# Performance work log

Measured on AMD Instinct MI355X. Metric: run time of the kernel, lower is better.

The kernel has to match this reference:

```python
import jax, jax.numpy as jnp
import numpy as np

L, H, NH, HD, F, B, S = 32, 1024, 16, 64, 2048, 2, 2048
HPH = H // NH  # hidden per attention head (hyena column split)
EPS = 1e-6
BLOCK = {0:'HCS',4:'HCS',7:'HCS',11:'HCS',14:'HCS',18:'HCS',21:'HCS',25:'HCS',28:'HCS',
         1:'HCM',5:'HCM',8:'HCM',12:'HCM',15:'HCM',19:'HCM',22:'HCM',26:'HCM',29:'HCM',
         2:'HCL',6:'HCL',9:'HCL',13:'HCL',16:'HCL',20:'HCL',23:'HCL',27:'HCL',30:'HCL',
         3:'ATT',10:'ATT',17:'ATT',24:'ATT',31:'ATT'}

def rmsnorm(x, w):
    return x * jax.lax.rsqrt(jnp.mean(x * x, -1, keepdims=True) + EPS) * w

def step_fir(u, state, w, b, flip=False, gated=False):
    # u:[B,C]  state:[B,C,cache]  w:[C,Lf]  b:[C]  (single-token FIR step)
    cache = state.shape[-1]
    w = w[:, ::-1][:, -(cache + 1):] if flip else w[:, :cache + 1]
    y = w[:, -1] * u + jnp.sum(state * w[:, :-1], -1)
    y = y + (b * u if gated else b)
    return y

def split3(z):
    # column_split_hyena=True path of _interleave_split
    r = z.reshape(z.shape[0], NH, 3 * HPH)
    x2 = r[:, :, :HPH].reshape(z.shape[0], H)
    x1 = r[:, :, HPH:2 * HPH].reshape(z.shape[0], H)
    v = r[:, :, 2 * HPH:].reshape(z.shape[0], H)
    return x2, x1, v

def mlp(x, W1, W2):
    return jax.nn.gelu(x @ W1.T) @ W2.T

def fir_block(x, n1, n2, pW, pb, oW, ob, W1, W2, sfw, sfb, h, D, fstate, istate, flip, gated):
    xn = rmsnorm(x, n1)
    z = xn @ pW.T + pb                 # [B,1,3H]
    u = z[:, -1]                       # [B,3H]
    zp = step_fir(u, fstate, sfw, sfb)
    x2, x1, v = split3(zp)
    y = step_fir(x1 * v, istate, h, D, flip=flip, gated=gated)
    y = (y * x2)[:, None]              # [B,1,H]
    x = y @ oW.T + ob + x
    return mlp(rmsnorm(x, n2), W1, W2) + x

def hcl_block(x, n1, n2, pW, pb, oW, ob, W1, W2, sfw, sfb, log_poles, residues, D, fstate, iir):
    xn = rmsnorm(x, n1)
    z = xn @ pW.T + pb
    u = z[:, -1]
    zp = step_fir(u, fstate, sfw, sfb)
    x2, x1, v = split3(zp)
    x1v = x1 * v
    iir_new = jnp.exp(log_poles) * iir + x1v[..., None]   # [B,H,SS] single-step IIR update
    res = jnp.sum(residues * iir_new, -1)
    y = (x2 * (res + D * x1v))[:, None]
    x = y @ oW.T + ob + x
    return mlp(rmsnorm(x, n2), W1, W2) + x

def att_block(x, n1, n2, qW, qb, oW, ob, W1, W2, kc, vc, cos, sin, pos):
    xn = rmsnorm(x, n1)
    qkv = (xn @ qW.T + qb).reshape(B, 1, 3, NH, HD)
    q, k, v = qkv[:, :, 0], qkv[:, :, 1], qkv[:, :, 2]
    c = jnp.concatenate([cos[pos], cos[pos]])  # [HD]
    s = jnp.concatenate([sin[pos], sin[pos]])
    rot = lambda t: jnp.concatenate([-t[..., HD // 2:], t[..., :HD // 2]], -1)
    q = q * c + rot(q) * s
    k = k * c + rot(k) * s
    kc = kc.at[:, pos].set(k[:, 0])  # KV-cache scatter write at current position
    vc = vc.at[:, pos].set(v[:, 0])
    scores = jnp.einsum('bohd,bshd->bhos', q, kc) * (HD ** -0.5)
    scores = jnp.where(jnp.arange(S) > pos, -10000.0, scores)
    aw = jax.nn.softmax(scores, -1)
    ctx = jnp.einsum('bhos,bshd->bohd', aw, vc).reshape(B, 1, H)
    x = ctx @ oW.T + ob + x
    return mlp(rmsnorm(x, n2), W1, W2) + x

def forward(x, position, norm1_w, norm2_w, proj_W, proj_b, out_W, out_b, mlp_W1, mlp_W2,
            sf_w, sf_b, hcs_h, hcs_D, hcm_h, hcm_D, hcl_logpoles, hcl_residues, hcl_D,
            fir_state, hcs_state, hcm_state, iir_state, k_cache, v_cache, rope_cos, rope_sin):
    att = 0
    for i in range(L):  # loop over 32 structurally distinct layers (static)
        t = BLOCK[i]
        cm = (norm1_w[i], norm2_w[i], proj_W[i], proj_b[i], out_W[i], out_b[i], mlp_W1[i], mlp_W2[i])
        if t == 'HCS':
            x = fir_block(x, *cm, sf_w[i], sf_b[i], hcs_h[i], hcs_D[i], fir_state[i], hcs_state[i], False, False)
        elif t == 'HCM':
            x = fir_block(x, *cm, sf_w[i], sf_b[i], hcm_h[i], hcm_D[i], fir_state[i], hcm_state[i], True, True)
        elif t == 'HCL':
            x = hcl_block(x, *cm, sf_w[i], sf_b[i], hcl_logpoles[i], hcl_residues[i], hcl_D[i], fir_state[i], iir_state[i])
        else:
            x = att_block(x, *cm, k_cache[att], v_cache[att], rope_cos, rope_sin, position)
            att += 1
    return x

def setup_inputs():
    key = jax.random.key(0)
    ks = jax.random.split(key, 24)
    g = lambda k, shape, sc: jax.random.normal(k, shape, jnp.float32) * sc
    inv_freq = 1.0 / (10000.0 ** (np.arange(0, HD, 2, dtype=np.float32) / HD))
    ang = np.arange(S, dtype=np.float32)[:, None] * inv_freq[None, :]
    return {
        'x': g(ks[0], (B, 1, H), 1.0),
        'position': 1024,
        'norm1_w': jnp.ones((L, H), jnp.float32),
        'norm2_w': jnp.ones((L, H), jnp.float32),
        'proj_W': g(ks[1], (L, 3 * H, H), H ** -0.5),
        'proj_b': jnp.zeros((L, 3 * H), jnp.float32),
        'out_W': g(ks[2], (L, H, H), 0.2 * H ** -0.5),
        'out_b': jnp.zeros((L, H), jnp.float32),
        'mlp_W1': g(ks[3], (L, F, H), H ** -0.5),
        'mlp_W2': g(ks[4], (L, H, F), 0.2 * F ** -0.5),
        'sf_w': g(ks[5], (L, 3 * H, 3), 0.4),
        'sf_b': g(ks[6], (L, 3 * H), 0.02),
        'hcs_h': g(ks[7], (L, H, 7), 0.2),
        'hcs_D': g(ks[8], (L, H), 0.2),
        'hcm_h': g(ks[9], (L, H, 128), 0.04),
        'hcm_D': g(ks[10], (L, H), 0.2),
        'hcl_logpoles': -jax.random.uniform(ks[11], (L, H, 16), jnp.float32, 0.01, 2.0),
        'hcl_residues': g(ks[12], (L, H, 16), 0.1),
        'hcl_D': g(ks[13], (L, H), 0.2),
        'fir_state': g(ks[14], (L, B, 3 * H, 2), 0.5),
        'hcs_state': g(ks[15], (L, B, H, 6), 0.5),
        'hcm_state': g(ks[16], (L, B, H, 127), 0.5),
        'iir_state': g(ks[17], (L, B, H, 16), 0.5),
        'k_cache': g(ks[18], (5, B, S, NH, HD), 1.0),
        'v_cache': g(ks[19], (5, B, S, NH, HD), 1.0),
        'rope_cos': jnp.asarray(np.cos(ang)),
        'rope_sin': jnp.asarray(np.sin(ang)),
    }

def reference(x, position, norm1_w, norm2_w, proj_W, proj_b, out_W, out_b, mlp_W1, mlp_W2,
              sf_w, sf_b, hcs_h, hcs_D, hcm_h, hcm_D, hcl_logpoles, hcl_residues, hcl_D,
              fir_state, hcs_state, hcm_state, iir_state, k_cache, v_cache, rope_cos, rope_sin):
    return forward(x, position, norm1_w, norm2_w, proj_W, proj_b, out_W, out_b, mlp_W1, mlp_W2,
                   sf_w, sf_b, hcs_h, hcs_D, hcm_h, hcm_D, hcl_logpoles, hcl_residues, hcl_D,
                   fir_state, hcs_state, hcm_state, iir_state, k_cache, v_cache, rope_cos, rope_sin)
```

## Files before the change

kernel.cpp:

```cpp
#include <hip/hip_runtime.h>
#include <hip/hip_bf16.h>
#include <math.h>

#define LAYERS 32
#define H      1024
#define H3     3072
#define NHEADS 16
#define HDIM   64
#define FF     2048
#define BATCH  2
#define SEQ    2048
#define EPSF   1e-6f

__device__ __forceinline__ float wredSum(float v) {
#pragma unroll
  for (int m = 32; m >= 1; m >>= 1) v += __shfl_xor(v, m, 64);
  return v;
}
__device__ __forceinline__ float wredMax(float v) {
#pragma unroll
  for (int m = 32; m >= 1; m >>= 1) v = fmaxf(v, __shfl_xor(v, m, 64));
  return v;
}
__device__ __forceinline__ float gelu_t(float x) {
  return 0.5f * x * (1.0f + tanhf(0.7978845608028654f * (x + 0.044715f * x * x * x)));
}
__device__ __forceinline__ float dot4(float4 a, float4 b) {
  return a.x * b.x + a.y * b.y + a.z * b.z + a.w * b.w;
}

__device__ __forceinline__ void ast(float* p, float v) {
  __hip_atomic_store(p, v, __ATOMIC_RELAXED, __HIP_MEMORY_SCOPE_AGENT);
}
__device__ __forceinline__ float ald(const float* p) {
  return __hip_atomic_load(p, __ATOMIC_RELAXED, __HIP_MEMORY_SCOPE_AGENT);
}
union F2U { unsigned long long u; float f[2]; };
__device__ __forceinline__ void ast2(unsigned long long* p, float lo, float hi) {
  F2U x; x.f[0] = lo; x.f[1] = hi;
  __hip_atomic_store(p, x.u, __ATOMIC_RELAXED, __HIP_MEMORY_SCOPE_AGENT);
}
__device__ __forceinline__ float2 ald2(const unsigned long long* p) {
  F2U x; x.u = __hip_atomic_load(p, __ATOMIC_RELAXED, __HIP_MEMORY_SCOPE_AGENT);
  return make_float2(x.f[0], x.f[1]);
}

__device__ __forceinline__ void slot_mark(int* slots, int idx) {
  __syncthreads();
  if (threadIdx.x == 0)
    __hip_atomic_store(&slots[idx], 1, __ATOMIC_RELAXED, __HIP_MEMORY_SCOPE_AGENT);
}
__device__ __forceinline__ void leader_detect(int* slots, int n, int* flags) {
  for (int s = threadIdx.x; s < n; s += 256) {
    while (__hip_atomic_load(&slots[s], __ATOMIC_RELAXED, __HIP_MEMORY_SCOPE_AGENT) == 0)
      __builtin_amdgcn_s_sleep(2);
  }
  __syncthreads();
  if (threadIdx.x < 8)
    __hip_atomic_store(&flags[threadIdx.x * 16], 1, __ATOMIC_RELAXED, __HIP_MEMORY_SCOPE_AGENT);
  asm volatile("" ::: "memory");
}
__device__ __forceinline__ void flag_wait(int* flags, int bid) {
  if (threadIdx.x == 0) {
    while (__hip_atomic_load(&flags[(bid & 7) * 16], __ATOMIC_RELAXED, __HIP_MEMORY_SCOPE_AGENT) == 0)
      __builtin_amdgcn_s_sleep(8);
  }
  __syncthreads();
  asm volatile("" ::: "memory");
}

union SH2 {
  struct { float xe[2048]; float red[8]; } ns;
  struct { float ys[2048]; float sml[512]; } mx;
  struct { float hs[4096]; } w2;
  struct { float q[64]; float k[64]; float v[64]; float eg[256]; float redA[4]; float osum[4][64]; } att;
};

__global__ __launch_bounds__(256, 6) void layer_k(
    int kind,
    const float* __restrict__ xin, float* __restrict__ xout,
    const float* __restrict__ n1L, const float* __restrict__ n2L,
    const float* __restrict__ pWL, const float* __restrict__ pbL,
    const float* __restrict__ oWL, const float* __restrict__ obL,
    const float* __restrict__ W1L, const float* __restrict__ W2L,
    const float* __restrict__ sfcL, const float* __restrict__ sfdL,
    const float* __restrict__ mix0L, const float* __restrict__ mix1L,
    const float* __restrict__ kcL, const float* __restrict__ vcL,
    const int* __restrict__ posp,
    const float* __restrict__ cosT, const float* __restrict__ sinT,
    unsigned long long* __restrict__ z2, float* __restrict__ attP,
    unsigned long long* __restrict__ xM2, unsigned long long* __restrict__ h2,
    int* __restrict__ barL)
{
  __shared__ SH2 sh;
  int bid = blockIdx.x, tid = threadIdx.x, lane = tid & 63, w = tid >> 6;
  int mixBase = (kind == 3) ? 1024 : 768;
  int w1Base  = (kind == 3) ? 1280 : 1024;
  int w2Base  = w1Base + 512;

  if (bid < 768) {
    float4 xv0 = ((const float4*)xin)[tid];
    float4 xv1 = ((const float4*)xin)[tid + 256];
    float4 nv  = ((const float4*)n1L)[tid];
    int r = bid * 4 + w;
    const float4* rowp = (const float4*)(pWL + (size_t)r * H);
    float4 wv0 = rowp[lane], wv1 = rowp[lane + 64],
           wv2 = rowp[lane + 128], wv3 = rowp[lane + 192];

    float ss0 = dot4(xv0, xv0), ss1 = dot4(xv1, xv1);
    ((float4*)sh.ns.xe)[tid]       = make_float4(xv0.x * nv.x, xv0.y * nv.y, xv0.z * nv.z, xv0.w * nv.w);
    ((float4*)sh.ns.xe)[tid + 256] = make_float4(xv1.x * nv.x, xv1.y * nv.y, xv1.z * nv.z, xv1.w * nv.w);
    ss0 = wredSum(ss0); ss1 = wredSum(ss1);
    if (lane == 0) { sh.ns.red[w] = ss0; sh.ns.red[4 + w] = ss1; }
    __syncthreads();
    float s0 = rsqrtf((sh.ns.red[0] + sh.ns.red[1] + sh.ns.red[2] + sh.ns.red[3]) * (1.0f / H) + EPSF);
    float s1 = rsqrtf((sh.ns.red[4] + sh.ns.red[5] + sh.ns.red[6] + sh.ns.red[7]) * (1.0f / H) + EPSF);

    const float4* x4 = (const float4*)sh.ns.xe;
    float a0 = dot4(wv0, x4[lane])       + dot4(wv1, x4[lane + 64])
             + dot4(wv2, x4[lane + 128]) + dot4(wv3, x4[lane + 192]);
    float a1 = dot4(wv0, x4[lane + 256]) + dot4(wv1, x4[lane + 320])
             + dot4(wv2, x4[lane + 384]) + dot4(wv3, x4[lane + 448]);
    a0 = wredSum(a0); a1 = wredSum(a1);
    if (lane == 0) {
      float b0 = pbL[r];
      ast2(&z2[r], a0 * s0 + b0, a1 * s1 + b0);
    }
    slot_mark(barL, bid);

  } else if (kind == 3 && bid < 1024) {
    int mb = bid - 768;
    int sp = mb & 7, n = (mb >> 3) & 15, b = mb >> 7;
    int pos = *posp;
    if (mb == 0) leader_detect(barL, 768, barL + 3072);
    else         flag_wait(barL + 3072, bid);
    if (tid < 64) {
      int d = tid, j = d & 31;
      float cs = cosT[pos * 32 + j], sn = sinT[pos * 32 + j];
      float2 zq  = ald2(&z2[n * 64 + d]);
      float2 zqo = ald2(&z2[n * 64 + ((d + 32) & 63)]);
      float2 zk  = ald2(&z2[1024 + n * 64 + d]);
      float2 zko = ald2(&z2[1024 + n * 64 + ((d + 32) & 63)]);
      float2 zv  = ald2(&z2[2048 + n * 64 + d]);
      float qv = b ? zq.y : zq.x,  qo = b ? zqo.y : zqo.x;
      float kv = b ? zk.y : zk.x,  ko = b ? zko.y : zko.x;
      sh.att.q[d] = ((d < 32) ? (qv * cs - qo * sn) : (qv * cs + qo * sn)) * 0.125f;
      sh.att.k[d] = (d < 32) ? (kv * cs - ko * sn) : (kv * cs + ko * sn);
      sh.att.v[d] = b ? zv.y : zv.x;
    }
    __syncthreads();
    int s = sp * 256 + tid;
    float logit = -1e30f;
    if (s <= pos) {
      const float4* k4 = (s == pos) ? (const float4*)sh.att.k
                                    : (const float4*)(kcL + (((size_t)b * SEQ + s) * NHEADS + n) * HDIM);
      const float4* q4 = (const float4*)sh.att.q;
      float acc = 0.f;
#pragma unroll
      for (int j = 0; j < 16; j++) acc += dot4(k4[j], q4[j]);
      logit = acc;
    }
    float m = wredMax(logit);
    if (lane == 0) sh.att.redA[w] = m;
    __syncthreads();
    m = fmaxf(fmaxf(sh.att.redA[0], sh.att.redA[1]), fmaxf(sh.att.redA[2], sh.att.redA[3]));
    float e = (s <= pos) ? expf(logit - m) : 0.f;
    sh.att.eg[tid] = e;
    float ps = wredSum(e);
    __syncthreads();
    if (lane == 0) sh.att.redA[w] = ps;
    __syncthreads();
    float lsum = sh.att.redA[0] + sh.att.redA[1] + sh.att.redA[2] + sh.att.redA[3];

    int dgrp = lane & 15, srow = lane >> 4;
    float4 acc = make_float4(0.f, 0.f, 0.f, 0.f);
#pragma unroll 4
    for (int it = 0; it < 16; it++) {
      int sl = w * 64 + it * 4;
      if (sp * 256 + sl > pos) break;
      int sli = sl + srow;
      int ss2 = sp * 256 + sli;
      float ev = sh.att.eg[sli];
      const float4* v4 = (ss2 == pos) ? (const float4*)sh.att.v
                                      : (const float4*)(vcL + (((size_t)b * SEQ + ss2) * NHEADS + n) * HDIM);
      float4 vv = v4[dgrp];
      acc.x += ev * vv.x; acc.y += ev * vv.y; acc.z += ev * vv.z; acc.w += ev * vv.w;
    }
#pragma unroll
    for (int mm = 16; mm <= 32; mm <<= 1) {
      acc.x += __shfl_xor(acc.x, mm, 64);
      acc.y += __shfl_xor(acc.y, mm, 64);
      acc.z += __shfl_xor(acc.z, mm, 64);
      acc.w += __shfl_xor(acc.w, mm, 64);
    }
    if (srow == 0) ((float4*)sh.att.osum[w])[dgrp] = acc;
    __syncthreads();
    float* Pp = attP + (size_t)((sp * BATCH + b) * NHEADS + n) * 66;
    if (tid < 64) ast(&Pp[tid], sh.att.osum[0][tid] + sh.att.osum[1][tid] + sh.att.osum[2][tid] + sh.att.osum[3][tid]);
    if (tid == 64) ast(&Pp[64], m);
    if (tid == 65) ast(&Pp[65], lsum);
    slot_mark(barL + 1024, mb);

  } else if (bid < w1Base) {
    int mb = bid - mixBase;
    int r = mb * 4 + w;
    const float4* rowp = (const float4*)(oWL + (size_t)r * H);
    float4 wv0 = rowp[lane], wv1 = rowp[lane + 64],
           wv2 = rowp[lane + 128], wv3 = rowp[lane + 192];

    if (kind != 3) {
      if (mb == 0) leader_detect(barL, 768, barL + 3200);
      else         flag_wait(barL + 3200, bid);
#pragma unroll
      for (int k = 0; k < 4; k++) {
        int c = tid + k * 256;
        int n = c >> 6, d = c & 63;
        int base = n * 192 + d;
        float2 za = ald2(&z2[base]);
        float2 zb = ald2(&z2[base + 64]);
        float2 zc = ald2(&z2[base + 128]);
        float x2a = sfcL[base] * za.x + sfdL[base];
        float x2b = sfcL[base] * za.y + sfdL[H3 + base];
        float x1a = sfcL[base + 64] * zb.x + sfdL[base + 64];
        float x1b = sfcL[base + 64] * zb.y + sfdL[H3 + base + 64];
        float va  = sfcL[base + 128] * zc.x + sfdL[base + 128];
        float vb  = sfcL[base + 128] * zc.y + sfdL[H3 + base + 128];
        sh.mx.ys[c]        = (mix1L[c] * (x1a * va) + mix0L[c]) * x2a;
        sh.mx.ys[1024 + c] = (mix1L[c] * (x1b * vb) + mix0L[H + c]) * x2b;
      }
    } else {
      if (mb == 0) leader_detect(barL + 1024, 256, barL + 3200);
      else         flag_wait(barL + 3200, bid);
      if (tid < 256) {
        int sp = tid & 7, n = (tid >> 3) & 15, b = tid >> 7;
        const float* Pp = attP + (size_t)((sp * BATCH + b) * NHEADS + n) * 66;
        sh.mx.sml[tid * 2] = ald(&Pp[64]);
        sh.mx.sml[tid * 2 + 1] = ald(&Pp[65]);
      }
      __syncthreads();
#pragma unroll
      for (int it = 0; it < 8; it++) {
        int e = tid + it * 256;
        int b = e >> 10, c = e & 1023;
        int n = c >> 6, d = c & 63;
        float M = -1e30f;
#pragma unroll
        for (int sp = 0; sp < 8; sp++) M = fmaxf(M, sh.mx.sml[(((b << 4) | n) * 8 + sp) * 2]);
        float Ls = 0.f, num = 0.f;
#pragma unroll
        for (int sp = 0; sp < 8; sp++) {
          float Msp = sh.mx.sml[(((b << 4) | n) * 8 + sp) * 2];
          float Lsp = sh.mx.sml[(((b << 4) | n) * 8 + sp) * 2 + 1];
          float wgt = expf(Msp - M);
          Ls += wgt * Lsp;
          num += wgt * ald(&attP[(size_t)((sp * BATCH + b) * NHEADS + n) * 66 + d]);
        }
        sh.mx.ys[e] = num / Ls;
      }
    }
    __syncthreads();
    const float4* y4 = (const float4*)sh.mx.ys;
    float a0 = dot4(wv0, y4[lane])       + dot4(wv1, y4[lane + 64])
             + dot4(wv2, y4[lane + 128]) + dot4(wv3, y4[lane + 192]);
    float a1 = dot4(wv0, y4[lane + 256]) + dot4(wv1, y4[lane + 320])
             + dot4(wv2, y4[lane + 384]) + dot4(wv3, y4[lane + 448]);
    a0 = wredSum(a0); a1 = wredSum(a1);
    if (lane == 0) {
      ast2(&xM2[r], a0 + obL[r] + xin[r], a1 + obL[r] + xin[H + r]);
    }
    slot_mark(barL + 1536, mb);

  } else if (bid < w2Base) {
    int wb = bid - w1Base;
    int r = wb * 4 + w;
    const float4* rowp = (const float4*)(W1L + (size_t)r * H);
    float4 wv0 = rowp[lane], wv1 = rowp[lane + 64],
           wv2 = rowp[lane + 128], wv3 = rowp[lane + 192];
    if (wb == 0) leader_detect(barL + 1536, 256, barL + 3328);
    else         flag_wait(barL + 3328, bid);

    float ss0 = 0.f, ss1 = 0.f;
#pragma unroll
    for (int k = 0; k < 4; k++) {
      int c = tid + k * 256;
      float2 xv = ald2(&xM2[c]);
      ss0 += xv.x * xv.x; ss1 += xv.y * xv.y;
      float nvj = n2L[c];
      sh.ns.xe[c] = xv.x * nvj;
      sh.ns.xe[1024 + c] = xv.y * nvj;
    }
    ss0 = wredSum(ss0); ss1 = wredSum(ss1);
    if (lane == 0) { sh.ns.red[w] = ss0; sh.ns.red[4 + w] = ss1; }
    __syncthreads();
    float s0 = rsqrtf((sh.ns.red[0] + sh.ns.red[1] + sh.ns.red[2] + sh.ns.red[3]) * (1.0f / H) + EPSF);
    float s1 = rsqrtf((sh.ns.red[4] + sh.ns.red[5] + sh.ns.red[6] + sh.ns.red[7]) * (1.0f / H) + EPSF);

    const float4* x4 = (const float4*)sh.ns.xe;
    float a0 = dot4(wv0, x4[lane])       + dot4(wv1, x4[lane + 64])
             + dot4(wv2, x4[lane + 128]) + dot4(wv3, x4[lane + 192]);
    float a1 = dot4(wv0, x4[lane + 256]) + dot4(wv1, x4[lane + 320])
             + dot4(wv2, x4[lane + 384]) + dot4(wv3, x4[lane + 448]);
    a0 = wredSum(a0); a1 = wredSum(a1);
    if (lane == 0) {
      ast2(&h2[r], gelu_t(a0 * s0), gelu_t(a1 * s1));
    }
    slot_mark(barL + 2048, wb);

  } else {
    int vb = bid - w2Base;
    int r = vb * 4 + w;
    const float4* rowp = (const float4*)(W2L + (size_t)r * FF);
    float4 wv[8];
#pragma unroll
    for (int j = 0; j < 8; j++) wv[j] = rowp[lane + 64 * j];
    if (vb == 0) leader_detect(barL + 2048, 512, barL + 3456);
    else         flag_wait(barL + 3456, bid);
#pragma unroll
    for (int it = 0; it < 8; it++) {
      int e = tid + it * 256;
      float2 hv = ald2(&h2[e]);
      sh.w2.hs[e] = hv.x;
      sh.w2.hs[2048 + e] = hv.y;
    }
    __syncthreads();
    const float4* h4 = (const float4*)sh.w2.hs;
    float a0 = 0.f, a1 = 0.f;
#pragma unroll
    for (int j = 0; j < 8; j++) {
      a0 += dot4(wv[j], h4[lane + 64 * j]);
      a1 += dot4(wv[j], h4[lane + 64 * j + 512]);
    }
    a0 = wredSum(a0); a1 = wredSum(a1);
    if (lane == 0) {
      float2 xm = ald2(&xM2[r]);
      xout[r]     = a0 + xm.x;
      xout[H + r] = a1 + xm.y;
    }
  }
}

__global__ __launch_bounds__(256) void prep_kernel(
    const float* __restrict__ sf_w, const float* __restrict__ sf_b,
    const float* __restrict__ fir_state,
    const float* __restrict__ hcs_h, const float* __restrict__ hcs_D, const float* __restrict__ hcs_state,
    const float* __restrict__ hcm_h, const float* __restrict__ hcm_D, const float* __restrict__ hcm_state,
    const float* __restrict__ lp, const float* __restrict__ resd, const float* __restrict__ hcl_D,
    const float* __restrict__ iir,
    unsigned long long kbits,
    float* __restrict__ sfd, float* __restrict__ sfc,
    float* __restrict__ mix0, float* __restrict__ mix1, int* __restrict__ bar)
{
  int blk = blockIdx.x, tid = threadIdx.x;
  if (blk < 768) {
    int idx = blk * 256 + tid;
    int i = idx / (BATCH * H3);
    int r = idx % (BATCH * H3);
    int b = r / H3, ch = r % H3;
    const float* fs = fir_state + ((size_t)(i * BATCH + b) * H3 + ch) * 2;
    const float* sw = sf_w + ((size_t)i * H3 + ch) * 3;
    sfd[idx] = fs[0] * sw[0] + fs[1] * sw[1] + sf_b[i * H3 + ch];
    if (b == 0) sfc[i * H3 + ch] = sw[2];
  } else if (blk < 1024) {
    int idx = (blk - 768) * 256 + tid;
    int i = idx >> 11;
    int r = idx & 2047;
    int b = r >> 10, c = r & 1023;
    int kind = (int)((kbits >> (2 * i)) & 3ull);
    if (kind == 0) {
      const float* st = hcs_state + ((size_t)(i * BATCH + b) * H + c) * 6;
      const float* hh = hcs_h + ((size_t)i * H + c) * 7;
      float acc = 0.f;
#pragma unroll
      for (int k = 0; k < 6; k++) acc += st[k] * hh[k];
      mix0[idx] = acc + hcs_D[i * H + c];
      if (b == 0) mix1[i * H + c] = hh[6];
    } else if (kind == 2) {
      const float* ii = iir + ((size_t)(i * BATCH + b) * H + c) * 16;
      const float* lpp = lp + ((size_t)i * H + c) * 16;
      const float* rs = resd + ((size_t)i * H + c) * 16;
      float acc = 0.f, rsum = 0.f;
#pragma unroll
      for (int k = 0; k < 16; k++) { float rv = rs[k]; acc += rv * expf(lpp[k]) * ii[k]; rsum += rv; }
      mix0[idx] = acc;
      if (b == 0) mix1[i * H + c] = rsum + hcl_D[i * H + c];
    }
  } else if (blk < 5632) {
    int w = tid >> 6, lane = tid & 63;
    int widx = (blk - 1024) * 4 + w;
    if (widx < 9 * BATCH * H) {
      int li = widx >> 11;
      int r = widx & 2047;
      int b = r >> 10, c = r & 1023;
      int i = (li >> 1) * 7 + ((li & 1) ? 5 : 1);
      const float* st = hcm_state + ((size_t)(i * BATCH + b) * H + c) * 127;
      const float* hh = hcm_h + ((size_t)i * H + c) * 128;
      float acc = 0.f;
      int k = lane;
      if (k < 127) acc += st[k] * hh[127 - k];
      k = lane + 64;
      if (k < 127) acc += st[k] * hh[127 - k];
      acc = wredSum(acc);
      if (lane == 0) {
        mix0[(i * BATCH + b) * H + c] = acc;
        if (b == 0) mix1[i * H + c] = hh[0] + hcm_D[i * H + c];
      }
    }
  } else {
    int idx = (blk - 5632) * 256 + tid;
    if (idx < LAYERS * 4096) bar[idx] = 0;
  }
}

extern "C" void kernel_launch(void* const* d_in, const int* in_sizes, int n_in,
                              void* d_out, int out_size, void* d_ws, size_t ws_size,
                              hipStream_t stream) {
  (void)in_sizes; (void)n_in; (void)out_size; (void)ws_size;
  const float* x0    = (const float*)d_in[0];
  const int*   posp  = (const int*)d_in[1];
  const float* n1    = (const float*)d_in[2];
  const float* n2    = (const float*)d_in[3];
  const float* pW    = (const float*)d_in[4];
  const float* pb    = (const float*)d_in[5];
  const float* oW    = (const float*)d_in[6];
  const float* ob    = (const float*)d_in[7];
  const float* W1    = (const float*)d_in[8];
  const float* W2    = (const float*)d_in[9];
  const float* sfw   = (const float*)d_in[10];
  const float* sfb   = (const float*)d_in[11];
  const float* hcs_h = (const float*)d_in[12];
  const float* hcs_D = (const float*)d_in[13];
  const float* hcm_h = (const float*)d_in[14];
  const float* hcm_D = (const float*)d_in[15];
  const float* lp    = (const float*)d_in[16];
  const float* resd  = (const float*)d_in[17];
  const float* hclD  = (const float*)d_in[18];
  const float* fir   = (const float*)d_in[19];
  const float* hcsS  = (const float*)d_in[20];
  const float* hcmS  = (const float*)d_in[21];
  const float* iir   = (const float*)d_in[22];
  const float* kc    = (const float*)d_in[23];
  const float* vc    = (const float*)d_in[24];
  const float* cosT  = (const float*)d_in[25];
  const float* sinT  = (const float*)d_in[26];

  float* ws    = (float*)d_ws;
  float* xbuf0 = ws;
  float* xbuf1 = ws + 2048;
  unsigned long long* xM2 = (unsigned long long*)(ws + 4096);
  unsigned long long* z2  = (unsigned long long*)(ws + 6144);
  unsigned long long* h2  = (unsigned long long*)(ws + 12288);
  float* attP  = ws + 16384;
  float* sfd   = ws + 33280;
  float* sfc   = ws + 229888;
  float* mix0  = ws + 328192;
  float* mix1  = ws + 393728;
  int*   bar   = (int*)(ws + 426496);

  static const int KIND[LAYERS] = {0,1,2,3,0,1,2,0,1,2,3,0,1,2,0,1,2,3,0,1,2,0,1,2,3,0,1,2,0,1,2,3};
  unsigned long long kbits = 0ull;
  for (int i = 0; i < LAYERS; i++) kbits |= ((unsigned long long)KIND[i]) << (2 * i);

  prep_kernel<<<6144, 256, 0, stream>>>(sfw, sfb, fir, hcs_h, hcs_D, hcsS,
      hcm_h, hcm_D, hcmS, lp, resd, hclD, iir, kbits, sfd, sfc, mix0, mix1, bar);

  const float* xsrc = x0;
  int att = 0;
  for (int i = 0; i < LAYERS; i++) {
    int kind = KIND[i];
    int nb = (kind == 3) ? 2048 : 1792;
    float* xout = (i == LAYERS - 1) ? (float*)d_out : ((i & 1) ? xbuf1 : xbuf0);
    const float* kcL = (kind == 3) ? kc + (size_t)att * BATCH * SEQ * NHEADS * HDIM : kc;
    const float* vcL = (kind == 3) ? vc + (size_t)att * BATCH * SEQ * NHEADS * HDIM : vc;
    layer_k<<<nb, 256, 0, stream>>>(
        kind, xsrc, xout,
        n1 + i * H, n2 + i * H,
        pW + (size_t)i * H3 * H, pb + i * H3,
        oW + (size_t)i * H * H, ob + i * H,
        W1 + (size_t)i * FF * H, W2 + (size_t)i * H * FF,
        sfc + (size_t)i * H3, sfd + (size_t)i * BATCH * H3,
        mix0 + (size_t)i * BATCH * H, mix1 + (size_t)i * H,
        kcL, vcL, posp, cosT, sinT,
        z2, attP, xM2, h2, bar + (size_t)i * 4096);
    if (kind == 3) att++;
    xsrc = xout;
  }
}
```

Before: 739.9 us.

## Fuse all 32 per-layer launches into one persistent mega-kernel with flag chaining

Replaces the host loop of 32 layer_k launches with a single launch of 32×2048 blocks. Each block derives its layer and kind from its block index. Layers are chained through device-side flags, so each layer's projection stage waits for the previous layer's W2 stage to finish. The residual stream is passed through ping-pong 64-bit interleaved buffers using atomic loads and stores. This removes per-launch overhead and lets weight rows for the next layer load before the dependency wait, overlapping memory traffic across layer boundaries. The costs are spinning waiter blocks that occupy CU slots, idle early-exit blocks in non-attention layers, and reliance on in-order block dispatch to avoid deadlock.

```diff
diff --git a/kernel.cpp b/kernel.cpp
--- a/kernel.cpp
+++ b/kernel.cpp
@@ -76,46 +76,62 @@
   struct { float q[64]; float k[64]; float v[64]; float eg[256]; float redA[4]; float osum[4][64]; } att;
 };
 
-__global__ __launch_bounds__(256, 6) void layer_k(
-    int kind,
-    const float* __restrict__ xin, float* __restrict__ xout,
-    const float* __restrict__ n1L, const float* __restrict__ n2L,
-    const float* __restrict__ pWL, const float* __restrict__ pbL,
-    const float* __restrict__ oWL, const float* __restrict__ obL,
-    const float* __restrict__ W1L, const float* __restrict__ W2L,
-    const float* __restrict__ sfcL, const float* __restrict__ sfdL,
-    const float* __restrict__ mix0L, const float* __restrict__ mix1L,
-    const float* __restrict__ kcL, const float* __restrict__ vcL,
-    const int* __restrict__ posp,
+__global__ __launch_bounds__(256, 8) void mega(
+    const float* __restrict__ x0, const int* __restrict__ posp,
+    const float* __restrict__ n1, const float* __restrict__ n2,
+    const float* __restrict__ pW, const float* __restrict__ pb,
+    const float* __restrict__ oW, const float* __restrict__ ob,
+    const float* __restrict__ W1, const float* __restrict__ W2,
+    const float* __restrict__ sfc, const float* __restrict__ sfd,
+    const float* __restrict__ mix0, const float* __restrict__ mix1,
+    const float* __restrict__ kc, const float* __restrict__ vc,
     const float* __restrict__ cosT, const float* __restrict__ sinT,
     unsigned long long* __restrict__ z2, float* __restrict__ attP,
     unsigned long long* __restrict__ xM2, unsigned long long* __restrict__ h2,
-    int* __restrict__ barL)
+    unsigned long long* __restrict__ xqA, unsigned long long* __restrict__ xqB,
+    int* __restrict__ bar, float* __restrict__ dout)
 {
   __shared__ SH2 sh;
   int bid = blockIdx.x, tid = threadIdx.x, lane = tid & 63, w = tid >> 6;
-  int mixBase = (kind == 3) ? 1024 : 768;
-  int w1Base  = (kind == 3) ? 1280 : 1024;
-  int w2Base  = w1Base + 512;
-
-  if (bid < 768) {
-    float4 xv0 = ((const float4*)xin)[tid];
-    float4 xv1 = ((const float4*)xin)[tid + 256];
-    float4 nv  = ((const float4*)n1L)[tid];
-    int r = bid * 4 + w;
-    const float4* rowp = (const float4*)(pWL + (size_t)r * H);
+  int layer = bid >> 11, local = bid & 2047;
+  int r7 = layer % 7;
+  int kind = (r7 == 3) ? 3 : ((r7 == 0 || r7 == 4) ? 0 : ((r7 == 1 || r7 == 5) ? 1 : 2));
+  int* barL = bar + layer * 4096;
+  unsigned long long* xr = (layer & 1) ? xqA : xqB;
+  unsigned long long* xw = (layer & 1) ? xqB : xqA;
+
+  if (local < 768) {
+    int r = local * 4 + w;
+    const float4* rowp = (const float4*)(pW + (size_t)layer * H3 * H + (size_t)r * H);
     float4 wv0 = rowp[lane], wv1 = rowp[lane + 64],
            wv2 = rowp[lane + 128], wv3 = rowp[lane + 192];
-
-    float ss0 = dot4(xv0, xv0), ss1 = dot4(xv1, xv1);
-    ((float4*)sh.ns.xe)[tid]       = make_float4(xv0.x * nv.x, xv0.y * nv.y, xv0.z * nv.z, xv0.w * nv.w);
-    ((float4*)sh.ns.xe)[tid + 256] = make_float4(xv1.x * nv.x, xv1.y * nv.y, xv1.z * nv.z, xv1.w * nv.w);
+    float4 nv = ((const float4*)(n1 + (size_t)layer * H))[tid];
+    if (layer > 0) {
+      if (local == 0) leader_detect(bar + (layer - 1) * 4096 + 2560, 256, barL + 3584);
+      else            flag_wait(barL + 3584, local);
+    }
+    float ss0 = 0.f, ss1 = 0.f;
+    if (layer == 0) {
+      float4 xv0 = ((const float4*)x0)[tid];
+      float4 xv1 = ((const float4*)x0)[tid + 256];
+      ss0 = dot4(xv0, xv0); ss1 = dot4(xv1, xv1);
+      ((float4*)sh.ns.xe)[tid]       = make_float4(xv0.x * nv.x, xv0.y * nv.y, xv0.z * nv.z, xv0.w * nv.w);
+      ((float4*)sh.ns.xe)[tid + 256] = make_float4(xv1.x * nv.x, xv1.y * nv.y, xv1.z * nv.z, xv1.w * nv.w);
+    } else {
+      float nn[4] = {nv.x, nv.y, nv.z, nv.w};
+#pragma unroll
+      for (int j = 0; j < 4; j++) {
+        float2 v = ald2(&xr[4 * tid + j]);
+        ss0 += v.x * v.x; ss1 += v.y * v.y;
+        sh.ns.xe[4 * tid + j] = v.x * nn[j];
+        sh.ns.xe[1024 + 4 * tid + j] = v.y * nn[j];
+      }
+    }
     ss0 = wredSum(ss0); ss1 = wredSum(ss1);
     if (lane == 0) { sh.ns.red[w] = ss0; sh.ns.red[4 + w] = ss1; }
     __syncthreads();
     float s0 = rsqrtf((sh.ns.red[0] + sh.ns.red[1] + sh.ns.red[2] + sh.ns.red[3]) * (1.0f / H) + EPSF);
     float s1 = rsqrtf((sh.ns.red[4] + sh.ns.red[5] + sh.ns.red[6] + sh.ns.red[7]) * (1.0f / H) + EPSF);
-
     const float4* x4 = (const float4*)sh.ns.xe;
     float a0 = dot4(wv0, x4[lane])       + dot4(wv1, x4[lane + 64])
              + dot4(wv2, x4[lane + 128]) + dot4(wv3, x4[lane + 192]);
@@ -123,17 +139,21 @@
              + dot4(wv2, x4[lane + 384]) + dot4(wv3, x4[lane + 448]);
     a0 = wredSum(a0); a1 = wredSum(a1);
     if (lane == 0) {
-      float b0 = pbL[r];
+      float b0 = pb[(size_t)layer * H3 + r];
       ast2(&z2[r], a0 * s0 + b0, a1 * s1 + b0);
     }
-    slot_mark(barL, bid);
-
-  } else if (kind == 3 && bid < 1024) {
-    int mb = bid - 768;
+    slot_mark(barL, local);
+
+  } else if (local < 1024) {
+    if (kind != 3) return;
+    int mb = local - 768;
     int sp = mb & 7, n = (mb >> 3) & 15, b = mb >> 7;
+    int att = layer / 7;
+    const float* kcL = kc + (size_t)att * BATCH * SEQ * NHEADS * HDIM;
+    const float* vcL = vc + (size_t)att * BATCH * SEQ * NHEADS * HDIM;
     int pos = *posp;
     if (mb == 0) leader_detect(barL, 768, barL + 3072);
-    else         flag_wait(barL + 3072, bid);
+    else         flag_wait(barL + 3072, local);
     if (tid < 64) {
       int d = tid, j = d & 31;
       float cs = cosT[pos * 32 + j], sn = sinT[pos * 32 + j];
@@ -171,7 +191,6 @@
     if (lane == 0) sh.att.redA[w] = ps;
     __syncthreads();
     float lsum = sh.att.redA[0] + sh.att.redA[1] + sh.att.redA[2] + sh.att.redA[3];
-
     int dgrp = lane & 15, srow = lane >> 4;
     float4 acc = make_float4(0.f, 0.f, 0.f, 0.f);
 #pragma unroll 4
@@ -201,16 +220,19 @@
     if (tid == 65) ast(&Pp[65], lsum);
     slot_mark(barL + 1024, mb);
 
-  } else if (bid < w1Base) {
-    int mb = bid - mixBase;
+  } else if (local < 1280) {
+    int mb = local - 1024;
     int r = mb * 4 + w;
-    const float4* rowp = (const float4*)(oWL + (size_t)r * H);
+    const float4* rowp = (const float4*)(oW + (size_t)layer * H * H + (size_t)r * H);
     float4 wv0 = rowp[lane], wv1 = rowp[lane + 64],
            wv2 = rowp[lane + 128], wv3 = rowp[lane + 192];
-
+    const float* sfcL = sfc + (size_t)layer * H3;
+    const float* sfdL = sfd + (size_t)layer * 2 * H3;
+    const float* mix0L = mix0 + (size_t)layer * 2 * H;
+    const float* mix1L = mix1 + (size_t)layer * H;
     if (kind != 3) {
       if (mb == 0) leader_detect(barL, 768, barL + 3200);
-      else         flag_wait(barL + 3200, bid);
+      else         flag_wait(barL + 3200, local);
 #pragma unroll
       for (int k = 0; k < 4; k++) {
         int c = tid + k * 256;
@@ -230,7 +252,7 @@
       }
     } else {
       if (mb == 0) leader_detect(barL + 1024, 256, barL + 3200);
-      else         flag_wait(barL + 3200, bid);
+      else         flag_wait(barL + 3200, local);
       if (tid < 256) {
         int sp = tid & 7, n = (tid >> 3) & 15, b = tid >> 7;
         const float* Pp = attP + (size_t)((sp * BATCH + b) * NHEADS + n) * 66;
@@ -266,26 +288,29 @@
              + dot4(wv2, y4[lane + 384]) + dot4(wv3, y4[lane + 448]);
     a0 = wredSum(a0); a1 = wredSum(a1);
     if (lane == 0) {
-      ast2(&xM2[r], a0 + obL[r] + xin[r], a1 + obL[r] + xin[H + r]);
+      float obv = ob[(size_t)layer * H + r];
+      float xi0, xi1;
+      if (layer == 0) { xi0 = x0[r]; xi1 = x0[H + r]; }
+      else { float2 t = ald2(&xr[r]); xi0 = t.x; xi1 = t.y; }
+      ast2(&xM2[r], a0 + obv + xi0, a1 + obv + xi1);
     }
     slot_mark(barL + 1536, mb);
 
-  } else if (bid < w2Base) {
-    int wb = bid - w1Base;
+  } else if (local < 1792) {
+    int wb = local - 1280;
     int r = wb * 4 + w;
-    const float4* rowp = (const float4*)(W1L + (size_t)r * H);
+    const float4* rowp = (const float4*)(W1 + (size_t)layer * FF * H + (size_t)r * H);
     float4 wv0 = rowp[lane], wv1 = rowp[lane + 64],
            wv2 = rowp[lane + 128], wv3 = rowp[lane + 192];
     if (wb == 0) leader_detect(barL + 1536, 256, barL + 3328);
-    else         flag_wait(barL + 3328, bid);
-
+    else         flag_wait(barL + 3328, local);
     float ss0 = 0.f, ss1 = 0.f;
 #pragma unroll
     for (int k = 0; k < 4; k++) {
       int c = tid + k * 256;
       float2 xv = ald2(&xM2[c]);
       ss0 += xv.x * xv.x; ss1 += xv.y * xv.y;
-      float nvj = n2L[c];
+      float nvj = n2[(size_t)layer * H + c];
       sh.ns.xe[c] = xv.x * nvj;
       sh.ns.xe[1024 + c] = xv.y * nvj;
     }
@@ -294,27 +319,24 @@
     __syncthreads();
     float s0 = rsqrtf((sh.ns.red[0] + sh.ns.red[1] + sh.ns.red[2] + sh.ns.red[3]) * (1.0f / H) + EPSF);
     float s1 = rsqrtf((sh.ns.red[4] + sh.ns.red[5] + sh.ns.red[6] + sh.ns.red[7]) * (1.0f / H) + EPSF);
-
     const float4* x4 = (const float4*)sh.ns.xe;
     float a0 = dot4(wv0, x4[lane])       + dot4(wv1, x4[lane + 64])
              + dot4(wv2, x4[lane + 128]) + dot4(wv3, x4[lane + 192]);
     float a1 = dot4(wv0, x4[lane + 256]) + dot4(wv1, x4[lane + 320])
              + dot4(wv2, x4[lane + 384]) + dot4(wv3, x4[lane + 448]);
     a0 = wredSum(a0); a1 = wredSum(a1);
-    if (lane == 0) {
-      ast2(&h2[r], gelu_t(a0 * s0), gelu_t(a1 * s1));
-    }
+    if (lane == 0) ast2(&h2[r], gelu_t(a0 * s0), gelu_t(a1 * s1));
     slot_mark(barL + 2048, wb);
 
   } else {
-    int vb = bid - w2Base;
+    int vb = local - 1792;
     int r = vb * 4 + w;
-    const float4* rowp = (const float4*)(W2L + (size_t)r * FF);
+    const float4* rowp = (const float4*)(W2 + (size_t)layer * H * FF + (size_t)r * FF);
     float4 wv[8];
 #pragma unroll
     for (int j = 0; j < 8; j++) wv[j] = rowp[lane + 64 * j];
     if (vb == 0) leader_detect(barL + 2048, 512, barL + 3456);
-    else         flag_wait(barL + 3456, bid);
+    else         flag_wait(barL + 3456, local);
 #pragma unroll
     for (int it = 0; it < 8; it++) {
       int e = tid + it * 256;
@@ -333,9 +355,14 @@
     a0 = wredSum(a0); a1 = wredSum(a1);
     if (lane == 0) {
       float2 xm = ald2(&xM2[r]);
-      xout[r]     = a0 + xm.x;
-      xout[H + r] = a1 + xm.y;
-    }
+      if (layer == LAYERS - 1) {
+        dout[r]     = a0 + xm.x;
+        dout[H + r] = a1 + xm.y;
+      } else {
+        ast2(&xw[r], a0 + xm.x, a1 + xm.y);
+      }
+    }
+    slot_mark(barL + 2560, vb);
   }
 }
 
@@ -444,8 +471,8 @@
   const float* sinT  = (const float*)d_in[26];
 
   float* ws    = (float*)d_ws;
-  float* xbuf0 = ws;
-  float* xbuf1 = ws + 2048;
+  unsigned long long* xqA = (unsigned long long*)ws;
+  unsigned long long* xqB = (unsigned long long*)(ws + 2048);
   unsigned long long* xM2 = (unsigned long long*)(ws + 4096);
   unsigned long long* z2  = (unsigned long long*)(ws + 6144);
   unsigned long long* h2  = (unsigned long long*)(ws + 12288);
@@ -463,25 +490,8 @@
   prep_kernel<<<6144, 256, 0, stream>>>(sfw, sfb, fir, hcs_h, hcs_D, hcsS,
       hcm_h, hcm_D, hcmS, lp, resd, hclD, iir, kbits, sfd, sfc, mix0, mix1, bar);
 
-  const float* xsrc = x0;
-  int att = 0;
-  for (int i = 0; i < LAYERS; i++) {
-    int kind = KIND[i];
-    int nb = (kind == 3) ? 2048 : 1792;
-    float* xout = (i == LAYERS - 1) ? (float*)d_out : ((i & 1) ? xbuf1 : xbuf0);
-    const float* kcL = (kind == 3) ? kc + (size_t)att * BATCH * SEQ * NHEADS * HDIM : kc;
-    const float* vcL = (kind == 3) ? vc + (size_t)att * BATCH * SEQ * NHEADS * HDIM : vc;
-    layer_k<<<nb, 256, 0, stream>>>(
-        kind, xsrc, xout,
-        n1 + i * H, n2 + i * H,
-        pW + (size_t)i * H3 * H, pb + i * H3,
-        oW + (size_t)i * H * H, ob + i * H,
-        W1 + (size_t)i * FF * H, W2 + (size_t)i * H * FF,
-        sfc + (size_t)i * H3, sfd + (size_t)i * BATCH * H3,
-        mix0 + (size_t)i * BATCH * H, mix1 + (size_t)i * H,
-        kcL, vcL, posp, cosT, sinT,
-        z2, attP, xM2, h2, bar + (size_t)i * 4096);
-    if (kind == 3) att++;
-    xsrc = xout;
-  }
-}
+  mega<<<LAYERS * 2048, 256, 0, stream>>>(
+      x0, posp, n1, n2, pW, pb, oW, ob, W1, W2,
+      sfc, sfd, mix0, mix1, kc, vc, cosT, sinT,
+      z2, attP, xM2, h2, xqA, xqB, bar, (float*)d_out);
+}
```

Result: slower. 1.127 ms (+52.4%).

## Fuse hyena mixing into projection blocks and replace leader barriers with byte-plane flags

Applied to the files above, without the earlier changes.

Non-attention layers now compute all three projection rows (x2, x1, v) for a channel inside one wave, apply the short FIR and the long-filter mix there, and write the gated y directly. This drops the separate z2 round trip and shrinks the grid from 1792 to 1280 blocks. The leader-detect/flag barrier is replaced by byte flags packed across 64 cache lines, which waiting blocks poll with a single wave-wide check, removing one serialized hop per stage. The trade-off is more weight registers per wave (three rows), a lower launch-bounds occupancy hint, and a polling scheme that depends on byte-store visibility.

```diff
diff --git a/kernel.cpp b/kernel.cpp
--- a/kernel.cpp
+++ b/kernel.cpp
@@ -11,6 +11,7 @@
 #define BATCH  2
 #define SEQ    2048
 #define EPSF   1e-6f
+#define LINE   128
 
 __device__ __forceinline__ float wredSum(float v) {
 #pragma unroll
@@ -45,25 +46,23 @@
   return make_float2(x.f[0], x.f[1]);
 }
 
-__device__ __forceinline__ void slot_mark(int* slots, int idx) {
+__device__ __forceinline__ void plane_mark(unsigned char* plane, int idx) {
   __syncthreads();
   if (threadIdx.x == 0)
-    __hip_atomic_store(&slots[idx], 1, __ATOMIC_RELAXED, __HIP_MEMORY_SCOPE_AGENT);
-}
-__device__ __forceinline__ void leader_detect(int* slots, int n, int* flags) {
-  for (int s = threadIdx.x; s < n; s += 256) {
-    while (__hip_atomic_load(&slots[s], __ATOMIC_RELAXED, __HIP_MEMORY_SCOPE_AGENT) == 0)
-      __builtin_amdgcn_s_sleep(2);
-  }
-  __syncthreads();
-  if (threadIdx.x < 8)
-    __hip_atomic_store(&flags[threadIdx.x * 16], 1, __ATOMIC_RELAXED, __HIP_MEMORY_SCOPE_AGENT);
-  asm volatile("" ::: "memory");
-}
-__device__ __forceinline__ void flag_wait(int* flags, int bid) {
-  if (threadIdx.x == 0) {
-    while (__hip_atomic_load(&flags[(bid & 7) * 16], __ATOMIC_RELAXED, __HIP_MEMORY_SCOPE_AGENT) == 0)
-      __builtin_amdgcn_s_sleep(8);
+    __hip_atomic_store(plane + (size_t)(idx & 63) * LINE + (idx >> 6),
+                       (unsigned char)0xFF, __ATOMIC_RELAXED, __HIP_MEMORY_SCOPE_AGENT);
+}
+template<int NDW>
+__device__ __forceinline__ void plane_wait(const unsigned char* plane) {
+  if (threadIdx.x < 64) {
+    const unsigned int* lp = (const unsigned int*)(plane + (size_t)threadIdx.x * LINE);
+    for (;;) {
+      bool ok = __hip_atomic_load(lp, __ATOMIC_RELAXED, __HIP_MEMORY_SCOPE_AGENT) == 0xFFFFFFFFu;
+      if (NDW > 1) ok &= __hip_atomic_load(lp + 1, __ATOMIC_RELAXED, __HIP_MEMORY_SCOPE_AGENT) == 0xFFFFFFFFu;
+      if (NDW > 2) ok &= __hip_atomic_load(lp + 2, __ATOMIC_RELAXED, __HIP_MEMORY_SCOPE_AGENT) == 0xFFFFFFFFu;
+      if (__all(ok)) break;
+      __builtin_amdgcn_s_sleep(4);
+    }
   }
   __syncthreads();
   asm volatile("" ::: "memory");
@@ -76,8 +75,8 @@
   struct { float q[64]; float k[64]; float v[64]; float eg[256]; float redA[4]; float osum[4][64]; } att;
 };
 
-__global__ __launch_bounds__(256, 6) void layer_k(
-    int kind,
+__global__ __launch_bounds__(256, 4) void layer_k(
+    int kind, int att,
     const float* __restrict__ xin, float* __restrict__ xout,
     const float* __restrict__ n1L, const float* __restrict__ n2L,
     const float* __restrict__ pWL, const float* __restrict__ pbL,
@@ -85,28 +84,45 @@
     const float* __restrict__ W1L, const float* __restrict__ W2L,
     const float* __restrict__ sfcL, const float* __restrict__ sfdL,
     const float* __restrict__ mix0L, const float* __restrict__ mix1L,
-    const float* __restrict__ kcL, const float* __restrict__ vcL,
+    const float* __restrict__ kc, const float* __restrict__ vc,
     const int* __restrict__ posp,
     const float* __restrict__ cosT, const float* __restrict__ sinT,
-    unsigned long long* __restrict__ z2, float* __restrict__ attP,
+    unsigned long long* __restrict__ z2, unsigned long long* __restrict__ y2,
+    float* __restrict__ attP,
     unsigned long long* __restrict__ xM2, unsigned long long* __restrict__ h2,
-    int* __restrict__ barL)
+    unsigned char* __restrict__ plane)
 {
   __shared__ SH2 sh;
-  int bid = blockIdx.x, tid = threadIdx.x, lane = tid & 63, w = tid >> 6;
-  int mixBase = (kind == 3) ? 1024 : 768;
-  int w1Base  = (kind == 3) ? 1280 : 1024;
+  int local = blockIdx.x, tid = threadIdx.x, lane = tid & 63, w = tid >> 6;
+  unsigned char* plP   = plane;
+  unsigned char* plAtt = plane + 8192;
+  unsigned char* plMix = plane + 16384;
+  unsigned char* plW1  = plane + 24576;
+  int isAtt = (kind == 3);
+  int mixBase = isAtt ? 1024 : 256;
+  int w1Base  = mixBase + 256;
   int w2Base  = w1Base + 512;
 
-  if (bid < 768) {
+  if (!isAtt && local < 256) {
+    int c0 = local * 4 + w;
+    int n = c0 >> 6, d = c0 & 63;
+    int R0 = n * 192 + d, R1 = R0 + 64, R2 = R0 + 128;
+    const float4* r0p = (const float4*)(pWL + (size_t)R0 * H);
+    const float4* r1p = (const float4*)(pWL + (size_t)R1 * H);
+    const float4* r2p = (const float4*)(pWL + (size_t)R2 * H);
+    float4 w0[4], w1v[4], w2v[4];
+#pragma unroll
+    for (int k = 0; k < 4; k++) { w0[k] = r0p[lane + 64 * k]; w1v[k] = r1p[lane + 64 * k]; w2v[k] = r2p[lane + 64 * k]; }
+    float pb0 = pbL[R0], pb1 = pbL[R1], pb2 = pbL[R2];
+    float sc0 = sfcL[R0], sc1 = sfcL[R1], sc2 = sfcL[R2];
+    float sd00 = sfdL[R0], sd10 = sfdL[H3 + R0];
+    float sd01 = sfdL[R1], sd11 = sfdL[H3 + R1];
+    float sd02 = sfdL[R2], sd12 = sfdL[H3 + R2];
+    float m0a = mix0L[c0], m0b = mix0L[H + c0], m1c = mix1L[c0];
+
     float4 xv0 = ((const float4*)xin)[tid];
     float4 xv1 = ((const float4*)xin)[tid + 256];
     float4 nv  = ((const float4*)n1L)[tid];
-    int r = bid * 4 + w;
-    const float4* rowp = (const float4*)(pWL + (size_t)r * H);
-    float4 wv0 = rowp[lane], wv1 = rowp[lane + 64],
-           wv2 = rowp[lane + 128], wv3 = rowp[lane + 192];
-
     float ss0 = dot4(xv0, xv0), ss1 = dot4(xv1, xv1);
     ((float4*)sh.ns.xe)[tid]       = make_float4(xv0.x * nv.x, xv0.y * nv.y, xv0.z * nv.z, xv0.w * nv.w);
     ((float4*)sh.ns.xe)[tid + 256] = make_float4(xv1.x * nv.x, xv1.y * nv.y, xv1.z * nv.z, xv1.w * nv.w);
@@ -115,7 +131,45 @@
     __syncthreads();
     float s0 = rsqrtf((sh.ns.red[0] + sh.ns.red[1] + sh.ns.red[2] + sh.ns.red[3]) * (1.0f / H) + EPSF);
     float s1 = rsqrtf((sh.ns.red[4] + sh.ns.red[5] + sh.ns.red[6] + sh.ns.red[7]) * (1.0f / H) + EPSF);
-
+    const float4* x4 = (const float4*)sh.ns.xe;
+    float a00 = 0.f, a01 = 0.f, a10 = 0.f, a11 = 0.f, a20 = 0.f, a21 = 0.f;
+#pragma unroll
+    for (int k = 0; k < 4; k++) {
+      float4 h0 = x4[lane + 64 * k], h1 = x4[lane + 64 * k + 256];
+      a00 += dot4(w0[k], h0);  a01 += dot4(w0[k], h1);
+      a10 += dot4(w1v[k], h0); a11 += dot4(w1v[k], h1);
+      a20 += dot4(w2v[k], h0); a21 += dot4(w2v[k], h1);
+    }
+    a00 = wredSum(a00); a01 = wredSum(a01);
+    a10 = wredSum(a10); a11 = wredSum(a11);
+    a20 = wredSum(a20); a21 = wredSum(a21);
+    if (lane == 0) {
+      float x2a = sc0 * (a00 * s0 + pb0) + sd00;
+      float x2b = sc0 * (a01 * s1 + pb0) + sd10;
+      float x1a = sc1 * (a10 * s0 + pb1) + sd01;
+      float x1b = sc1 * (a11 * s1 + pb1) + sd11;
+      float va  = sc2 * (a20 * s0 + pb2) + sd02;
+      float vb  = sc2 * (a21 * s1 + pb2) + sd12;
+      ast2(&y2[c0], (m1c * (x1a * va) + m0a) * x2a, (m1c * (x1b * vb) + m0b) * x2b);
+    }
+    plane_mark(plP, local);
+
+  } else if (isAtt && local < 768) {
+    int r = local * 4 + w;
+    const float4* rowp = (const float4*)(pWL + (size_t)r * H);
+    float4 wv0 = rowp[lane], wv1 = rowp[lane + 64],
+           wv2 = rowp[lane + 128], wv3 = rowp[lane + 192];
+    float4 xv0 = ((const float4*)xin)[tid];
+    float4 xv1 = ((const float4*)xin)[tid + 256];
+    float4 nv  = ((const float4*)n1L)[tid];
+    float ss0 = dot4(xv0, xv0), ss1 = dot4(xv1, xv1);
+    ((float4*)sh.ns.xe)[tid]       = make_float4(xv0.x * nv.x, xv0.y * nv.y, xv0.z * nv.z, xv0.w * nv.w);
+    ((float4*)sh.ns.xe)[tid + 256] = make_float4(xv1.x * nv.x, xv1.y * nv.y, xv1.z * nv.z, xv1.w * nv.w);
+    ss0 = wredSum(ss0); ss1 = wredSum(ss1);
+    if (lane == 0) { sh.ns.red[w] = ss0; sh.ns.red[4 + w] = ss1; }
+    __syncthreads();
+    float s0 = rsqrtf((sh.ns.red[0] + sh.ns.red[1] + sh.ns.red[2] + sh.ns.red[3]) * (1.0f / H) + EPSF);
+    float s1 = rsqrtf((sh.ns.red[4] + sh.ns.red[5] + sh.ns.red[6] + sh.ns.red[7]) * (1.0f / H) + EPSF);
     const float4* x4 = (const float4*)sh.ns.xe;
     float a0 = dot4(wv0, x4[lane])       + dot4(wv1, x4[lane + 64])
              + dot4(wv2, x4[lane + 128]) + dot4(wv3, x4[lane + 192]);
@@ -126,14 +180,15 @@
       float b0 = pbL[r];
       ast2(&z2[r], a0 * s0 + b0, a1 * s1 + b0);
     }
-    slot_mark(barL, bid);
-
-  } else if (kind == 3 && bid < 1024) {
-    int mb = bid - 768;
+    plane_mark(plP, local);
+
+  } else if (isAtt && local < 1024) {
+    int mb = local - 768;
     int sp = mb & 7, n = (mb >> 3) & 15, b = mb >> 7;
+    const float* kcL = kc + (size_t)att * BATCH * SEQ * NHEADS * HDIM;
+    const float* vcL = vc + (size_t)att * BATCH * SEQ * NHEADS * HDIM;
     int pos = *posp;
-    if (mb == 0) leader_detect(barL, 768, barL + 3072);
-    else         flag_wait(barL + 3072, bid);
+    plane_wait<3>(plP);
     if (tid < 64) {
       int d = tid, j = d & 31;
       float cs = cosT[pos * 32 + j], sn = sinT[pos * 32 + j];
@@ -171,7 +226,6 @@
     if (lane == 0) sh.att.redA[w] = ps;
     __syncthreads();
     float lsum = sh.att.redA[0] + sh.att.redA[1] + sh.att.redA[2] + sh.att.redA[3];
-
     int dgrp = lane & 15, srow = lane >> 4;
     float4 acc = make_float4(0.f, 0.f, 0.f, 0.f);
 #pragma unroll 4
@@ -199,38 +253,25 @@
     if (tid < 64) ast(&Pp[tid], sh.att.osum[0][tid] + sh.att.osum[1][tid] + sh.att.osum[2][tid] + sh.att.osum[3][tid]);
     if (tid == 64) ast(&Pp[64], m);
     if (tid == 65) ast(&Pp[65], lsum);
-    slot_mark(barL + 1024, mb);
-
-  } else if (bid < w1Base) {
-    int mb = bid - mixBase;
+    plane_mark(plAtt, mb);
+
+  } else if (local < w1Base) {
+    int mb = local - mixBase;
     int r = mb * 4 + w;
     const float4* rowp = (const float4*)(oWL + (size_t)r * H);
     float4 wv0 = rowp[lane], wv1 = rowp[lane + 64],
            wv2 = rowp[lane + 128], wv3 = rowp[lane + 192];
-
-    if (kind != 3) {
-      if (mb == 0) leader_detect(barL, 768, barL + 3200);
-      else         flag_wait(barL + 3200, bid);
+    if (!isAtt) {
+      plane_wait<1>(plP);
 #pragma unroll
       for (int k = 0; k < 4; k++) {
         int c = tid + k * 256;
-        int n = c >> 6, d = c & 63;
-        int base = n * 192 + d;
-        float2 za = ald2(&z2[base]);
-        float2 zb = ald2(&z2[base + 64]);
-        float2 zc = ald2(&z2[base + 128]);
-        float x2a = sfcL[base] * za.x + sfdL[base];
-        float x2b = sfcL[base] * za.y + sfdL[H3 + base];
-        float x1a = sfcL[base + 64] * zb.x + sfdL[base + 64];
-        float x1b = sfcL[base + 64] * zb.y + sfdL[H3 + base + 64];
-        float va  = sfcL[base + 128] * zc.x + sfdL[base + 128];
-        float vb  = sfcL[base + 128] * zc.y + sfdL[H3 + base + 128];
-        sh.mx.ys[c]        = (mix1L[c] * (x1a * va) + mix0L[c]) * x2a;
-        sh.mx.ys[1024 + c] = (mix1L[c] * (x1b * vb) + mix0L[H + c]) * x2b;
+        float2 t = ald2(&y2[c]);
+        sh.mx.ys[c] = t.x;
+        sh.mx.ys[1024 + c] = t.y;
       }
     } else {
-      if (mb == 0) leader_detect(barL + 1024, 256, barL + 3200);
-      else         flag_wait(barL + 3200, bid);
+      plane_wait<1>(plAtt);
       if (tid < 256) {
         int sp = tid & 7, n = (tid >> 3) & 15, b = tid >> 7;
         const float* Pp = attP + (size_t)((sp * BATCH + b) * NHEADS + n) * 66;
@@ -266,19 +307,18 @@
              + dot4(wv2, y4[lane + 384]) + dot4(wv3, y4[lane + 448]);
     a0 = wredSum(a0); a1 = wredSum(a1);
     if (lane == 0) {
-      ast2(&xM2[r], a0 + obL[r] + xin[r], a1 + obL[r] + xin[H + r]);
-    }
-    slot_mark(barL + 1536, mb);
-
-  } else if (bid < w2Base) {
-    int wb = bid - w1Base;
+      float obv = obL[r];
+      ast2(&xM2[r], a0 + obv + xin[r], a1 + obv + xin[H + r]);
+    }
+    plane_mark(plMix, mb);
+
+  } else if (local < w2Base) {
+    int wb = local - w1Base;
     int r = wb * 4 + w;
     const float4* rowp = (const float4*)(W1L + (size_t)r * H);
     float4 wv0 = rowp[lane], wv1 = rowp[lane + 64],
            wv2 = rowp[lane + 128], wv3 = rowp[lane + 192];
-    if (wb == 0) leader_detect(barL + 1536, 256, barL + 3328);
-    else         flag_wait(barL + 3328, bid);
-
+    plane_wait<1>(plMix);
     float ss0 = 0.f, ss1 = 0.f;
 #pragma unroll
     for (int k = 0; k < 4; k++) {
@@ -294,27 +334,23 @@
     __syncthreads();
     float s0 = rsqrtf((sh.ns.red[0] + sh.ns.red[1] + sh.ns.red[2] + sh.ns.red[3]) * (1.0f / H) + EPSF);
     float s1 = rsqrtf((sh.ns.red[4] + sh.ns.red[5] + sh.ns.red[6] + sh.ns.red[7]) * (1.0f / H) + EPSF);
-
     const float4* x4 = (const float4*)sh.ns.xe;
     float a0 = dot4(wv0, x4[lane])       + dot4(wv1, x4[lane + 64])
              + dot4(wv2, x4[lane + 128]) + dot4(wv3, x4[lane + 192]);
     float a1 = dot4(wv0, x4[lane + 256]) + dot4(wv1, x4[lane + 320])
              + dot4(wv2, x4[lane + 384]) + dot4(wv3, x4[lane + 448]);
     a0 = wredSum(a0); a1 = wredSum(a1);
-    if (lane == 0) {
-      ast2(&h2[r], gelu_t(a0 * s0), gelu_t(a1 * s1));
-    }
-    slot_mark(barL + 2048, wb);
+    if (lane == 0) ast2(&h2[r], gelu_t(a0 * s0), gelu_t(a1 * s1));
+    plane_mark(plW1, wb);
 
   } else {
-    int vb = bid - w2Base;
+    int vb = local - w2Base;
     int r = vb * 4 + w;
     const float4* rowp = (const float4*)(W2L + (size_t)r * FF);
     float4 wv[8];
 #pragma unroll
     for (int j = 0; j < 8; j++) wv[j] = rowp[lane + 64 * j];
-    if (vb == 0) leader_detect(barL + 2048, 512, barL + 3456);
-    else         flag_wait(barL + 3456, bid);
+    plane_wait<2>(plW1);
 #pragma unroll
     for (int it = 0; it < 8; it++) {
       int e = tid + it * 256;
@@ -358,7 +394,7 @@
     int b = r / H3, ch = r % H3;
     const float* fs = fir_state + ((size_t)(i * BATCH + b) * H3 + ch) * 2;
     const float* sw = sf_w + ((size_t)i * H3 + ch) * 3;
-    sfd[idx] = fs[0] * sw[0] + fs[1] * sw[1] + sf_b[i * H3 + ch];
+    sfd[(size_t)i * 2 * H3 + b * H3 + ch] = fs[0] * sw[0] + fs[1] * sw[1] + sf_b[i * H3 + ch];
     if (b == 0) sfc[i * H3 + ch] = sw[2];
   } else if (blk < 1024) {
     int idx = (blk - 768) * 256 + tid;
@@ -407,7 +443,7 @@
     }
   } else {
     int idx = (blk - 5632) * 256 + tid;
-    if (idx < LAYERS * 4096) bar[idx] = 0;
+    if (idx < LAYERS * 8192) bar[idx] = 0;
   }
 }
 
@@ -446,41 +482,42 @@
   float* ws    = (float*)d_ws;
   float* xbuf0 = ws;
   float* xbuf1 = ws + 2048;
-  unsigned long long* xM2 = (unsigned long long*)(ws + 4096);
+  unsigned long long* y2  = (unsigned long long*)(ws + 4096);
   unsigned long long* z2  = (unsigned long long*)(ws + 6144);
-  unsigned long long* h2  = (unsigned long long*)(ws + 12288);
-  float* attP  = ws + 16384;
-  float* sfd   = ws + 33280;
-  float* sfc   = ws + 229888;
-  float* mix0  = ws + 328192;
-  float* mix1  = ws + 393728;
-  int*   bar   = (int*)(ws + 426496);
+  unsigned long long* xM2 = (unsigned long long*)(ws + 12288);
+  unsigned long long* h2  = (unsigned long long*)(ws + 14336);
+  float* attP  = ws + 18432;
+  float* sfd   = ws + 35328;
+  float* sfc   = ws + 231936;
+  float* mix0  = ws + 330240;
+  float* mix1  = ws + 395776;
+  int*   bar   = (int*)(ws + 428544);
 
   static const int KIND[LAYERS] = {0,1,2,3,0,1,2,0,1,2,3,0,1,2,0,1,2,3,0,1,2,0,1,2,3,0,1,2,0,1,2,3};
   unsigned long long kbits = 0ull;
   for (int i = 0; i < LAYERS; i++) kbits |= ((unsigned long long)KIND[i]) << (2 * i);
 
-  prep_kernel<<<6144, 256, 0, stream>>>(sfw, sfb, fir, hcs_h, hcs_D, hcsS,
+  int zblocks = (LAYERS * 8192 + 255) / 256;
+  prep_kernel<<<5632 + zblocks, 256, 0, stream>>>(sfw, sfb, fir, hcs_h, hcs_D, hcsS,
       hcm_h, hcm_D, hcmS, lp, resd, hclD, iir, kbits, sfd, sfc, mix0, mix1, bar);
 
   const float* xsrc = x0;
   int att = 0;
   for (int i = 0; i < LAYERS; i++) {
     int kind = KIND[i];
-    int nb = (kind == 3) ? 2048 : 1792;
+    int nb = (kind == 3) ? 2048 : 1280;
     float* xout = (i == LAYERS - 1) ? (float*)d_out : ((i & 1) ? xbuf1 : xbuf0);
-    const float* kcL = (kind == 3) ? kc + (size_t)att * BATCH * SEQ * NHEADS * HDIM : kc;
-    const float* vcL = (kind == 3) ? vc + (size_t)att * BATCH * SEQ * NHEADS * HDIM : vc;
     layer_k<<<nb, 256, 0, stream>>>(
-        kind, xsrc, xout,
-        n1 + i * H, n2 + i * H,
-        pW + (size_t)i * H3 * H, pb + i * H3,
-        oW + (size_t)i * H * H, ob + i * H,
+        kind, att, xsrc, xout,
+        n1 + (size_t)i * H, n2 + (size_t)i * H,
+        pW + (size_t)i * H3 * H, pb + (size_t)i * H3,
+        oW + (size_t)i * H * H, ob + (size_t)i * H,
         W1 + (size_t)i * FF * H, W2 + (size_t)i * H * FF,
-        sfc + (size_t)i * H3, sfd + (size_t)i * BATCH * H3,
-        mix0 + (size_t)i * BATCH * H, mix1 + (size_t)i * H,
-        kcL, vcL, posp, cosT, sinT,
-        z2, attP, xM2, h2, bar + (size_t)i * 4096);
+        sfc + (size_t)i * H3, sfd + (size_t)i * 2 * H3,
+        mix0 + (size_t)i * 2 * H, mix1 + (size_t)i * H,
+        kc, vc, posp, cosT, sinT,
+        z2, y2, attP, xM2, h2,
+        (unsigned char*)(bar + (size_t)i * 8192));
     if (kind == 3) att++;
     xsrc = xout;
   }
```

After: 886.7 us. +19.8%, slower.
